# Kernel tuning notes

Hardware: AMD Instinct MI355X
Metric: run time of the kernel (lower is better)

The kernel has to match this reference:

```python
import jax, jax.numpy as jnp
import numpy as np

D_MODEL = 1024
D_STATE = 16
EXPAND = 2
D_INNER = EXPAND * D_MODEL
DT_RANK = 64  # ceil(1024/16)
D_CONV = 4


def setup_inputs() -> dict:
    key = jax.random.key(0)
    ks = jax.random.split(key, 8)
    s = 0.02
    x = jax.random.normal(ks[0], (2, 2048, D_MODEL), dtype=jnp.float32)
    W_in = jax.random.normal(ks[1], (D_MODEL, 2 * D_INNER), dtype=jnp.float32) * s
    W_conv = jax.random.normal(ks[2], (D_CONV, D_INNER), dtype=jnp.float32) * s  # depthwise taps
    b_conv = jnp.zeros((D_INNER,), dtype=jnp.float32)
    W_xproj = jax.random.normal(ks[3], (D_INNER, DT_RANK + 2 * D_STATE), dtype=jnp.float32) * s
    W_dt = jax.random.normal(ks[4], (DT_RANK, D_INNER), dtype=jnp.float32) * s
    b_dt = jnp.zeros((D_INNER,), dtype=jnp.float32)
    A_log = jnp.broadcast_to(jnp.log(jnp.arange(1, D_STATE + 1, dtype=jnp.float32)), (D_INNER, D_STATE))
    D = jnp.ones((D_INNER,), dtype=jnp.float32)
    W_out = jax.random.normal(ks[5], (D_INNER, D_MODEL), dtype=jnp.float32) * s
    return {"x": x, "W_in": W_in, "W_conv": W_conv, "b_conv": b_conv,
            "W_xproj": W_xproj, "W_dt": W_dt, "b_dt": b_dt,
            "A_log": A_log, "D": D, "W_out": W_out}


def _silu(v):
    return v * jax.nn.sigmoid(v)


def reference(x, W_in, W_conv, b_conv, W_xproj, W_dt, b_dt, A_log, D, W_out):
    B_, L, _ = x.shape
    xz = x @ W_in                     # [B, L, 2*d_inner]
    x_in, z = jnp.split(xz, 2, axis=-1)
    # causal depthwise conv1d (torch padding=d_conv-1 then slice to seq_len)
    pad = D_CONV - 1
    x_pad = jnp.pad(x_in, ((0, 0), (pad, 0), (0, 0)))
    x_conv = b_conv
    x_conv = sum(x_pad[:, k:k + L, :] * W_conv[k] for k in range(D_CONV)) + b_conv
    x_in = _silu(x_conv)              # [B, L, d_inner]
    dbc = x_in @ W_xproj
    dt = jax.nn.softplus(dbc[..., :DT_RANK] @ W_dt + b_dt)   # [B, L, d_inner]
    Bm = dbc[..., DT_RANK:DT_RANK + D_STATE]                  # [B, L, d_state]
    Cm = dbc[..., DT_RANK + D_STATE:]                          # [B, L, d_state]
    A = -jnp.exp(A_log)                                        # [d_inner, d_state]

    def step(state, inp):
        x_t, dt_t, B_t, C_t = inp   # [B,d_inner], [B,d_inner], [B,d_state], [B,d_state]
        dA = jnp.exp(jnp.clip(dt_t[:, :, None] * A[None], -10.0, 10.0))
        dB = dt_t[:, :, None] * B_t[:, None, :]
        state = jnp.clip(state * dA + x_t[:, :, None] * dB, -10.0, 10.0)
        y_t = jnp.einsum('bdn,bn->bd', state, C_t) + D * x_t
        return state, y_t

    tm = lambda a: jnp.swapaxes(a, 0, 1)  # time-major
    state0 = jnp.zeros((B_, D_INNER, D_STATE), dtype=x.dtype)
    _, ys = jax.lax.scan(step, state0, (tm(x_in), tm(dt), tm(Bm), tm(Cm)))
    y = jnp.swapaxes(ys, 0, 1)            # [B, L, d_inner]
    y = y * _silu(z)
    return y @ W_out                       # [B, L, d_model]
```

## Files before the change

kernel.cpp:

```cpp
#include <hip/hip_runtime.h>
#include <math.h>

#define D_MODEL 1024
#define D_INNER 2048
#define D_STATE 16
#define DT_RANK 64
#define LSEQ 2048
#define NBATCH 2
#define M_TOT (NBATCH * LSEQ)
#define DBC_STRIDE 128
#define CH 64
#define NCH (LSEQ / CH)
#define KSPL 8
#define OKSPL 2

typedef unsigned short ushort_t;
typedef unsigned int uint_t;
typedef __attribute__((ext_vector_type(8))) short bf16x8;
typedef __attribute__((ext_vector_type(4))) float f32x4;

__device__ __forceinline__ ushort_t f2bf_rne(float f) {
    uint_t u = __float_as_uint(f);
    u += 0x7fffu + ((u >> 16) & 1u);
    return (ushort_t)(u >> 16);
}
__device__ __forceinline__ float bf2f(ushort_t h) {
    return __uint_as_float(((uint_t)h) << 16);
}
__device__ __forceinline__ float fexp2(float x) {
#if __has_builtin(__builtin_amdgcn_exp2f)
    return __builtin_amdgcn_exp2f(x);
#else
    return exp2f(x);
#endif
}
__device__ __forceinline__ float frcp(float x) {
#if __has_builtin(__builtin_amdgcn_rcpf)
    return __builtin_amdgcn_rcpf(x);
#else
    return 1.f / x;
#endif
}
__device__ __forceinline__ float clip10(float x) {
#if __has_builtin(__builtin_amdgcn_fmed3f)
    return __builtin_amdgcn_fmed3f(x, -10.f, 10.f);
#else
    return fminf(fmaxf(x, -10.f), 10.f);
#endif
}

#define LOG2E 1.44269504f
#define NLOG2E10 -14.4269504f

#define KIN 1024
#define KTI (KIN / 64)

#define BAR()   __builtin_amdgcn_s_barrier()
#define LGKM0() asm volatile("s_waitcnt lgkmcnt(0)" ::: "memory")

#define LDFRAG_B(SRC)                                                          \
    _Pragma("unroll")                                                          \
    for (int nf = 0; nf < 4; ++nf)                                             \
        fB[nf] = *reinterpret_cast<const bf16x8*>(                             \
            &(SRC)[(bRow + nf * 16 + fm) * 32 + swz * 8]);

#define LDFRAG_A(SRC, MOFF)                                                    \
    _Pragma("unroll")                                                          \
    for (int mf = 0; mf < 4; ++mf)                                             \
        fA[mf] = *reinterpret_cast<const bf16x8*>(                             \
            &(SRC)[(aRow + (MOFF + mf) * 16 + fm) * 32 + swz * 8]);

#define MFMA_QUAD(MOFF)                                                        \
    __builtin_amdgcn_s_setprio(1);                                             \
    _Pragma("unroll")                                                          \
    for (int mf = 0; mf < 4; ++mf)                                             \
        _Pragma("unroll")                                                      \
        for (int nf = 0; nf < 4; ++nf)                                         \
            acc[MOFF + mf][nf] = __builtin_amdgcn_mfma_f32_16x16x32_bf16(      \
                fA[mf], fB[nf], acc[MOFF + mf][nf], 0, 0, 0);                  \
    __builtin_amdgcn_s_setprio(0);

__global__ __launch_bounds__(512, 2) void gemm256_inproj(
    const ushort_t* __restrict__ Ah, const ushort_t* __restrict__ BTh,
    float* __restrict__ C, float* __restrict__ AUX)
{
    __shared__ __align__(1024) ushort_t smem[65536];
    const int tid  = threadIdx.x;
    const int lane = tid & 63;
    const int w    = tid >> 6;
    const int wm   = w >> 2;
    const int wn   = w & 3;
    const int fm   = lane & 15, fk = lane >> 4;
    const int swz  = fk ^ ((fm >> 1) & 3);
    const int aRow = wm * 128;
    const int bRow = wn * 64;
    const int m0   = blockIdx.y * 256;
    const int n0   = blockIdx.x * 256;
    const int rbase = w * 16 + (lane >> 2);
    const int ssw   = ((lane & 3) ^ ((lane >> 3) & 3)) * 8;

    f32x4 acc[8][4] = {};

    auto stage = [&](const ushort_t* __restrict__ g, int grow0, int kcol,
                     int regUS) {
        #pragma unroll
        for (int q = 0; q < 2; ++q) {
            const ushort_t* src =
                g + (size_t)(grow0 + q * 128 + rbase) * KIN + kcol + ssw;
            __builtin_amdgcn_global_load_lds(
                (const __attribute__((address_space(1))) void*)src,
                (__attribute__((address_space(3))) void*)(smem + regUS +
                                                          q * 4096 + w * 512),
                16, 0, 0);
        }
    };

    stage(Ah,  m0, 0,  0);
    stage(BTh, n0, 0,  32768);
    stage(Ah,  m0, 32, 8192);
    stage(BTh, n0, 32, 32768 + 8192);
    stage(Ah,  m0, 64, 16384);
    stage(BTh, n0, 64, 32768 + 16384);
    asm volatile("s_waitcnt vmcnt(8)" ::: "memory");
    BAR();

    bf16x8 fA[4], fB[4];

    for (int t = 0; t < KTI - 1; ++t) {
        const int bf = t & 1, bn = bf ^ 1;
        const ushort_t* A0 = smem + (bf * 2 + 0) * 8192;
        const ushort_t* A1 = smem + (bf * 2 + 1) * 8192;
        const ushort_t* B0 = smem + 32768 + (bf * 2 + 0) * 8192;
        const ushort_t* B1 = smem + 32768 + (bf * 2 + 1) * 8192;
        const int kc1 = (t + 1) * 64, kc2 = (t + 2) * 64;
        const bool st2 = (t + 2 < KTI);

        LDFRAG_B(B0);
        LDFRAG_A(A0, 0);
        stage(Ah, m0, kc1 + 32, (bn * 2 + 1) * 8192);
        BAR(); LGKM0();
        MFMA_QUAD(0);
        BAR();

        LDFRAG_A(A0, 4);
        stage(BTh, n0, kc1 + 32, 32768 + (bn * 2 + 1) * 8192);
        BAR(); LGKM0();
        MFMA_QUAD(4);
        asm volatile("s_waitcnt vmcnt(8)" ::: "memory");
        BAR();
        __builtin_amdgcn_sched_barrier(0);

        LDFRAG_B(B1);
        LDFRAG_A(A1, 0);
        if (st2) stage(Ah, m0, kc2, (bf * 2 + 0) * 8192);
        BAR(); LGKM0();
        MFMA_QUAD(0);
        BAR();

        LDFRAG_A(A1, 4);
        if (st2) stage(BTh, n0, kc2, 32768 + (bf * 2 + 0) * 8192);
        BAR(); LGKM0();
        MFMA_QUAD(4);
        if (t == KTI - 2) { asm volatile("s_waitcnt vmcnt(4)" ::: "memory"); }
        else              { asm volatile("s_waitcnt vmcnt(6)" ::: "memory"); }
        BAR();
        __builtin_amdgcn_sched_barrier(0);
    }

    {
        const int bf = (KTI - 1) & 1;
        const ushort_t* A0 = smem + (bf * 2 + 0) * 8192;
        const ushort_t* A1 = smem + (bf * 2 + 1) * 8192;
        const ushort_t* B0 = smem + 32768 + (bf * 2 + 0) * 8192;
        const ushort_t* B1 = smem + 32768 + (bf * 2 + 1) * 8192;

        LDFRAG_B(B0);
        LDFRAG_A(A0, 0);
        BAR(); LGKM0();
        MFMA_QUAD(0);
        BAR();

        LDFRAG_A(A0, 4);
        BAR(); LGKM0();
        MFMA_QUAD(4);
        asm volatile("s_waitcnt vmcnt(0)" ::: "memory");
        BAR();

        LDFRAG_B(B1);
        LDFRAG_A(A1, 0);
        BAR(); LGKM0();
        MFMA_QUAD(0);
        BAR();

        LDFRAG_A(A1, 4);
        BAR(); LGKM0();
        MFMA_QUAD(4);
    }

    float* dst = (n0 < D_INNER) ? C : AUX;
    const int csub = (n0 < D_INNER) ? 0 : D_INNER;
    #pragma unroll
    for (int mf = 0; mf < 8; ++mf) {
        int row0 = m0 + aRow + mf * 16 + fk * 4;
        #pragma unroll
        for (int nf = 0; nf < 4; ++nf) {
            int col = n0 + bRow + nf * 16 + fm - csub;
            #pragma unroll
            for (int r = 0; r < 4; ++r)
                dst[(size_t)(row0 + r) * D_INNER + col] = acc[mf][nf][r];
        }
    }
}

template <int MODE, int TERMS>
__global__ __launch_bounds__(256) void gemm_bf16s(
    const ushort_t* __restrict__ Ah, const ushort_t* __restrict__ Al,
    const ushort_t* __restrict__ BTh, const ushort_t* __restrict__ BTl,
    float* __restrict__ C, float* __restrict__ AUX, int M, int N, int K)
{
    __shared__ __align__(16) ushort_t smem[4 * 128 * 32];
    ushort_t* sAh = smem;
    ushort_t* sAl = smem + 4096;
    ushort_t* sBh = smem + 8192;
    ushort_t* sBl = smem + 12288;
    const int tid = threadIdx.x;
    const int lane = tid & 63;
    const int m0 = blockIdx.y * 128;
    int ks = 0, nblk = blockIdx.x;
    if (MODE == 3) { ks = blockIdx.x; nblk = 0; }
    if (MODE == 4) { ks = blockIdx.x >> 3; nblk = blockIdx.x & 7; }
    const int n0 = nblk * 128;
    const int wave = tid >> 6;
    const int mw = (wave & 1) * 64, nw = (wave >> 1) * 64;
    const int fm = lane & 15, fk = lane >> 4;
    const int swz = fk ^ ((fm >> 1) & 3);

    f32x4 acc[4][4] = {};

    const int r_st0 = tid >> 2, cp0 = tid & 3;
    const int r_st1 = (256 + tid) >> 2, cp1 = tid & 3;
    const int cl0 = cp0 ^ ((r_st0 >> 1) & 3);
    const int cl1 = cp1 ^ ((r_st1 >> 1) & 3);
    const int ldsb0 = (tid & ~63) * 16;
    const int ldsb1 = (256 + (tid & ~63)) * 16;

    const int kbeg = (MODE == 3) ? ks * (K / KSPL)
                   : (MODE == 4) ? ks * (K / OKSPL) : 0;
    const int kend = (MODE == 3) ? kbeg + K / KSPL
                   : (MODE == 4) ? kbeg + K / OKSPL : K;

    for (int k0 = kbeg; k0 < kend; k0 += 32) {
        __syncthreads();
        {
            size_t ga0 = (size_t)(m0 + r_st0) * K + k0 + cl0 * 8;
            size_t ga1 = (size_t)(m0 + r_st1) * K + k0 + cl1 * 8;
            size_t gb0 = (size_t)(n0 + r_st0) * K + k0 + cl0 * 8;
            size_t gb1 = (size_t)(n0 + r_st1) * K + k0 + cl1 * 8;
            __builtin_amdgcn_global_load_lds(
                (const __attribute__((address_space(1))) void*)(Ah + ga0),
                (__attribute__((address_space(3))) void*)((char*)sAh + ldsb0), 16, 0, 0);
            __builtin_amdgcn_global_load_lds(
                (const __attribute__((address_space(1))) void*)(Ah + ga1),
                (__attribute__((address_space(3))) void*)((char*)sAh + ldsb1), 16, 0, 0);
            if (TERMS >= 3) {
                __builtin_amdgcn_global_load_lds(
                    (const __attribute__((address_space(1))) void*)(Al + ga0),
                    (__attribute__((address_space(3))) void*)((char*)sAl + ldsb0), 16, 0, 0);
                __builtin_amdgcn_global_load_lds(
                    (const __attribute__((address_space(1))) void*)(Al + ga1),
                    (__attribute__((address_space(3))) void*)((char*)sAl + ldsb1), 16, 0, 0);
            }
            __builtin_amdgcn_global_load_lds(
                (const __attribute__((address_space(1))) void*)(BTh + gb0),
                (__attribute__((address_space(3))) void*)((char*)sBh + ldsb0), 16, 0, 0);
            __builtin_amdgcn_global_load_lds(
                (const __attribute__((address_space(1))) void*)(BTh + gb1),
                (__attribute__((address_space(3))) void*)((char*)sBh + ldsb1), 16, 0, 0);
            if (TERMS >= 2) {
                __builtin_amdgcn_global_load_lds(
                    (const __attribute__((address_space(1))) void*)(BTl + gb0),
                    (__attribute__((address_space(3))) void*)((char*)sBl + ldsb0), 16, 0, 0);
                __builtin_amdgcn_global_load_lds(
                    (const __attribute__((address_space(1))) void*)(BTl + gb1),
                    (__attribute__((address_space(3))) void*)((char*)sBl + ldsb1), 16, 0, 0);
            }
        }
        __syncthreads();

        bf16x8 fAh[4], fAl[4], fBh[4], fBl[4];
        #pragma unroll
        for (int t = 0; t < 4; ++t) {
            int ra = (mw + t * 16 + fm) * 32 + swz * 8;
            int rb = (nw + t * 16 + fm) * 32 + swz * 8;
            fAh[t] = *reinterpret_cast<const bf16x8*>(&sAh[ra]);
            if (TERMS >= 3) fAl[t] = *reinterpret_cast<const bf16x8*>(&sAl[ra]);
            fBh[t] = *reinterpret_cast<const bf16x8*>(&sBh[rb]);
            if (TERMS >= 2) fBl[t] = *reinterpret_cast<const bf16x8*>(&sBl[rb]);
        }
        #pragma unroll
        for (int i = 0; i < 4; ++i)
            #pragma unroll
            for (int j = 0; j < 4; ++j) {
                acc[i][j] = __builtin_amdgcn_mfma_f32_16x16x32_bf16(fAh[i], fBh[j], acc[i][j], 0, 0, 0);
                if (TERMS >= 3)
                    acc[i][j] = __builtin_amdgcn_mfma_f32_16x16x32_bf16(fAl[i], fBh[j], acc[i][j], 0, 0, 0);
                if (TERMS >= 2)
                    acc[i][j] = __builtin_amdgcn_mfma_f32_16x16x32_bf16(fAh[i], fBl[j], acc[i][j], 0, 0, 0);
            }
    }

    float* Cq = (MODE == 3 || MODE == 4) ? C + (size_t)ks * M * N : C;
    #pragma unroll
    for (int i = 0; i < 4; ++i) {
        int row0 = m0 + mw + i * 16 + fk * 4;
        #pragma unroll
        for (int j = 0; j < 4; ++j) {
            int col = n0 + nw + j * 16 + fm;
            if (MODE == 5) {
                const float* bias = (const float*)AUX;
                float bc_ = bias[col];
                #pragma unroll
                for (int r = 0; r < 4; ++r) {
                    float t = acc[i][j][r] + bc_;
                    C[(size_t)(row0 + r) * N + col] =
                        fmaxf(t, 0.f) + log1pf(__expf(-fabsf(t)));
                }
            } else {
                #pragma unroll
                for (int r = 0; r < 4; ++r)
                    Cq[(size_t)(row0 + r) * N + col] = acc[i][j][r];
            }
        }
    }
}

__global__ __launch_bounds__(256) void xproj_red_k(
    const float* __restrict__ dbcp, float* __restrict__ dbc,
    ushort_t* __restrict__ dbch)
{
    int g = blockIdx.x * 256 + threadIdx.x;
    int m = g >> 7, c = g & 127;
    float s = 0.f;
    #pragma unroll
    for (int ks = 0; ks < KSPL; ++ks)
        s += dbcp[(size_t)ks * M_TOT * DBC_STRIDE + g];
    dbc[g] = s;
    if (c < 64)
        dbch[(size_t)m * 64 + c] = f2bf_rne(s);
}

__global__ __launch_bounds__(256) void outred_k(
    const float* __restrict__ p, float* __restrict__ out)
{
    int i4 = (blockIdx.x * 256 + threadIdx.x) * 4;
    f32x4 a = *reinterpret_cast<const f32x4*>(p + i4);
    f32x4 b = *reinterpret_cast<const f32x4*>(p + (size_t)M_TOT * D_MODEL + i4);
    *reinterpret_cast<f32x4*>(out + i4) = a + b;
}

__global__ __launch_bounds__(256) void cast_h_k(
    const float* __restrict__ X, ushort_t* __restrict__ Xh)
{
    int i4 = (blockIdx.x * 256 + threadIdx.x) * 4;
    float4 v = *reinterpret_cast<const float4*>(X + i4);
    ushort2 a = make_ushort2(f2bf_rne(v.x), f2bf_rne(v.y));
    ushort2 b = make_ushort2(f2bf_rne(v.z), f2bf_rne(v.w));
    *reinterpret_cast<ushort2*>(Xh + i4)     = a;
    *reinterpret_cast<ushort2*>(Xh + i4 + 2) = b;
}

__global__ __launch_bounds__(256) void transpose_cast_k(
    const float* __restrict__ W, ushort_t* __restrict__ Th, ushort_t* __restrict__ Tl,
    int K, int N)
{
    __shared__ float tile[32][33];
    int n0 = blockIdx.x * 32, k0 = blockIdx.y * 32;
    int tx = threadIdx.x & 31, ty = threadIdx.x >> 5;
    #pragma unroll
    for (int i = 0; i < 32; i += 8)
        tile[ty + i][tx] = W[(size_t)(k0 + ty + i) * N + n0 + tx];
    __syncthreads();
    #pragma unroll
    for (int i = 0; i < 32; i += 8) {
        float v = tile[tx][ty + i];
        ushort_t h = f2bf_rne(v);
        ushort_t l = f2bf_rne(v - bf2f(h));
        size_t o = (size_t)(n0 + ty + i) * K + k0 + tx;
        Th[o] = h; Tl[o] = l;
    }
}

__global__ __launch_bounds__(256) void transpose_cast_pad_k(
    const float* __restrict__ W, ushort_t* __restrict__ Th, int K, int N)
{
    __shared__ float tile[32][33];
    int n0 = blockIdx.x * 32, k0 = blockIdx.y * 32;
    int tx = threadIdx.x & 31, ty = threadIdx.x >> 5;
    #pragma unroll
    for (int i = 0; i < 32; i += 8)
        tile[ty + i][tx] = (n0 + tx < N) ? W[(size_t)(k0 + ty + i) * N + n0 + tx] : 0.f;
    __syncthreads();
    #pragma unroll
    for (int i = 0; i < 32; i += 8) {
        float v = tile[tx][ty + i];
        size_t o = (size_t)(n0 + ty + i) * K + k0 + tx;
        Th[o] = f2bf_rne(v);
    }
}

__global__ __launch_bounds__(256) void conv_silu_k(
    const float* __restrict__ xbuf, const float* __restrict__ Wc,
    const float* __restrict__ bc, ushort_t* __restrict__ xinh,
    float* __restrict__ xf)
{
    __shared__ float tile[67][64];
    const int c0 = blockIdx.x * 64;
    const int m0 = blockIdx.y * 64;
    const int bstart = m0 & ~(LSEQ - 1);
    const int tid = threadIdx.x;

    for (int e = tid; e < 67 * 64; e += 256) {
        int r = e >> 6, c = e & 63;
        int g = m0 - 3 + r;
        tile[r][c] = (g >= bstart) ? xbuf[(size_t)g * D_INNER + c0 + c] : 0.f;
    }
    __syncthreads();

    const int c_l = tid & 63, mg = tid >> 6;
    const int c = c0 + c_l;
    const float w0 = Wc[c], w1 = Wc[D_INNER + c];
    const float w2 = Wc[2 * D_INNER + c], w3 = Wc[3 * D_INNER + c];
    const float bb = bc[c];
    #pragma unroll
    for (int mi = 0; mi < 16; ++mi) {
        int r = mg * 16 + mi;
        float acc = bb + tile[r][c_l] * w0 + tile[r + 1][c_l] * w1
                       + tile[r + 2][c_l] * w2 + tile[r + 3][c_l] * w3;
        float sv = acc / (1.f + __expf(-acc));
        xinh[(size_t)(m0 + r) * D_INNER + c] = f2bf_rne(sv);
        xf[(size_t)(m0 + r) * D_INNER + c] = sv;
    }
}

__global__ __launch_bounds__(256) void scan_sum_k2(
    const float* __restrict__ dtf, const float* __restrict__ xf,
    const float* __restrict__ dbc, const float* __restrict__ A_log,
    float* __restrict__ asumb, float* __restrict__ sendb)
{
    __shared__ float sdt[16][256];
    __shared__ float sx[16][256];
    __shared__ float sB[16][16];
    const int tid = threadIdx.x;
    const int lane = tid & 63;
    const int w = tid >> 6;
    const int c0 = blockIdx.x << 8;
    const int ck = blockIdx.y;
    const int b  = blockIdx.z;
    const size_t mbase = (size_t)b * LSEQ + (size_t)ck * CH;
    const int d = c0 + tid;

    float AdnL2[16];
    #pragma unroll
    for (int n = 0; n < 16; ++n)
        AdnL2[n] = -__expf(A_log[d * D_STATE + n]) * LOG2E;

    float s[16] = {};
    float asum[16] = {};

    for (int tt = 0; tt < CH / 16; ++tt) {
        const size_t rowm = mbase + tt * 16;
        __syncthreads();
        #pragma unroll
        for (int p = 0; p < 4; ++p) {
            const int r = w + p * 4;
            const size_t g = (rowm + r) * D_INNER + c0 + lane * 4;
            __builtin_amdgcn_global_load_lds(
                (const __attribute__((address_space(1))) void*)(dtf + g),
                (__attribute__((address_space(3))) void*)(&sdt[r][0]), 16, 0, 0);
            __builtin_amdgcn_global_load_lds(
                (const __attribute__((address_space(1))) void*)(xf + g),
                (__attribute__((address_space(3))) void*)(&sx[r][0]), 16, 0, 0);
        }
        if (w == 0) {
            const int r = lane >> 2, c4 = (lane & 3) * 4;
            __builtin_amdgcn_global_load_lds(
                (const __attribute__((address_space(1))) void*)(
                    dbc + (rowm + r) * DBC_STRIDE + 64 + c4),
                (__attribute__((address_space(3))) void*)(&sB[0][0]), 16, 0, 0);
        }
        __syncthreads();

        #pragma unroll 2
        for (int t = 0; t < 16; ++t) {
            const float dv = sdt[t][tid];
            const float xv = sx[t][tid];
            const float p  = dv * xv;
            const f32x4 B0 = *reinterpret_cast<const f32x4*>(&sB[t][0]);
            const f32x4 B1 = *reinterpret_cast<const f32x4*>(&sB[t][4]);
            const f32x4 B2 = *reinterpret_cast<const f32x4*>(&sB[t][8]);
            const f32x4 B3 = *reinterpret_cast<const f32x4*>(&sB[t][12]);
            #pragma unroll
            for (int n = 0; n < 16; ++n) {
                const float Bn = (n < 4) ? B0[n] : (n < 8) ? B1[n - 4]
                               : (n < 12) ? B2[n - 8] : B3[n - 12];
                float a = fmaxf(dv * AdnL2[n], NLOG2E10);
                asum[n] += a;
                float e = fexp2(a);
                s[n] = clip10(fmaf(s[n], e, p * Bn));
            }
        }
    }
    #pragma unroll
    for (int n = 0; n < 16; ++n) {
        size_t o = (((size_t)(b * NCH + ck) * 16) + n) * D_INNER + d;
        asumb[o] = asum[n];
        sendb[o] = s[n];
    }
}

__global__ __launch_bounds__(256) void scan_fix_k2(
    const float* __restrict__ asumb, const float* __restrict__ sendb,
    float* __restrict__ sinb)
{
    int g = blockIdx.x * 256 + threadIdx.x;
    int d = g & (D_INNER - 1);
    int n = (g >> 11) & 15;
    int b = g >> 15;
    float s = 0.f;
    for (int ck = 0; ck < NCH; ++ck) {
        size_t idx = (((size_t)(b * NCH + ck) * 16) + n) * D_INNER + d;
        sinb[idx] = s;
        s = clip10(fmaf(s, fexp2(asumb[idx]), sendb[idx]));
    }
}

__global__ __launch_bounds__(256) void scan_apply_k2(
    const float* __restrict__ dtf, const float* __restrict__ xf,
    const float* __restrict__ dbc, const float* __restrict__ zf,
    const float* __restrict__ sinb, const float* __restrict__ A_log,
    const float* __restrict__ Dv, ushort_t* __restrict__ Yh)
{
    __shared__ float sdt[16][256];
    __shared__ float sx[16][256];
    __shared__ float sz[16][256];
    __shared__ float sBC[16][32];
    const int tid = threadIdx.x;
    const int lane = tid & 63;
    const int w = tid >> 6;
    const int c0 = blockIdx.x << 8;
    const int ck = blockIdx.y;
    const int b  = blockIdx.z;
    const size_t mbase = (size_t)b * LSEQ + (size_t)ck * CH;
    const int d = c0 + tid;

    float AdnL2[16];
    #pragma unroll
    for (int n = 0; n < 16; ++n)
        AdnL2[n] = -__expf(A_log[d * D_STATE + n]) * LOG2E;
    const float Dd = Dv[d];

    float s[16];
    #pragma unroll
    for (int n = 0; n < 16; ++n)
        s[n] = sinb[(((size_t)(b * NCH + ck) * 16) + n) * D_INNER + d];

    for (int tt = 0; tt < CH / 16; ++tt) {
        const size_t rowm = mbase + tt * 16;
        __syncthreads();
        #pragma unroll
        for (int p = 0; p < 4; ++p) {
            const int r = w + p * 4;
            const size_t g = (rowm + r) * D_INNER + c0 + lane * 4;
            __builtin_amdgcn_global_load_lds(
                (const __attribute__((address_space(1))) void*)(dtf + g),
                (__attribute__((address_space(3))) void*)(&sdt[r][0]), 16, 0, 0);
            __builtin_amdgcn_global_load_lds(
                (const __attribute__((address_space(1))) void*)(xf + g),
                (__attribute__((address_space(3))) void*)(&sx[r][0]), 16, 0, 0);
            __builtin_amdgcn_global_load_lds(
                (const __attribute__((address_space(1))) void*)(zf + g),
                (__attribute__((address_space(3))) void*)(&sz[r][0]), 16, 0, 0);
        }
        if (w < 2) {
            const int r = tid >> 3, c8 = (tid & 7) * 4;
            __builtin_amdgcn_global_load_lds(
                (const __attribute__((address_space(1))) void*)(
                    dbc + (rowm + r) * DBC_STRIDE + 64 + c8),
                (__attribute__((address_space(3))) void*)(&sBC[w * 8][0]), 16, 0, 0);
        }
        __syncthreads();

        #pragma unroll 2
        for (int t = 0; t < 16; ++t) {
            const float dv = sdt[t][tid];
            const float xv = sx[t][tid];
            const float p  = dv * xv;
            const f32x4 B0 = *reinterpret_cast<const f32x4*>(&sBC[t][0]);
            const f32x4 B1 = *reinterpret_cast<const f32x4*>(&sBC[t][4]);
            const f32x4 B2 = *reinterpret_cast<const f32x4*>(&sBC[t][8]);
            const f32x4 B3 = *reinterpret_cast<const f32x4*>(&sBC[t][12]);
            const f32x4 C0 = *reinterpret_cast<const f32x4*>(&sBC[t][16]);
            const f32x4 C1 = *reinterpret_cast<const f32x4*>(&sBC[t][20]);
            const f32x4 C2 = *reinterpret_cast<const f32x4*>(&sBC[t][24]);
            const f32x4 C3 = *reinterpret_cast<const f32x4*>(&sBC[t][28]);
            float y = Dd * xv;
            #pragma unroll
            for (int n = 0; n < 16; ++n) {
                const float Bn = (n < 4) ? B0[n] : (n < 8) ? B1[n - 4]
                               : (n < 12) ? B2[n - 8] : B3[n - 12];
                const float Cn = (n < 4) ? C0[n] : (n < 8) ? C1[n - 4]
                               : (n < 12) ? C2[n - 8] : C3[n - 12];
                float a = fmaxf(dv * AdnL2[n], NLOG2E10);
                float e = fexp2(a);
                s[n] = clip10(fmaf(s[n], e, p * Bn));
                y = fmaf(s[n], Cn, y);
            }
            const float zz = sz[t][tid];
            const float gate = zz * frcp(1.f + fexp2(zz * -LOG2E));
            Yh[(rowm + t) * D_INNER + d] = f2bf_rne(y * gate);
        }
    }
}

extern "C" void kernel_launch(void* const* d_in, const int* in_sizes, int n_in,
                              void* d_out, int out_size, void* d_ws, size_t ws_size,
                              hipStream_t stream)
{
    const float* x       = (const float*)d_in[0];
    const float* W_in    = (const float*)d_in[1];
    const float* W_conv  = (const float*)d_in[2];
    const float* b_conv  = (const float*)d_in[3];
    const float* W_xproj = (const float*)d_in[4];
    const float* W_dt    = (const float*)d_in[5];
    const float* b_dt    = (const float*)d_in[6];
    const float* A_log   = (const float*)d_in[7];
    const float* Dv      = (const float*)d_in[8];
    const float* W_out   = (const float*)d_in[9];
    float* out = (float*)d_out;

    float* xbuf = (float*)d_ws;
    float* zf   = xbuf + (size_t)M_TOT * D_INNER;
    float* dbc  = zf + (size_t)M_TOT * D_INNER;
    float* BCT  = dbc + (size_t)M_TOT * DBC_STRIDE;
    ushort_t* xh     = (ushort_t*)(BCT + (size_t)32 * M_TOT);
    ushort_t* xl     = xh + (size_t)M_TOT * D_MODEL;
    ushort_t* WinTh  = xl + (size_t)M_TOT * D_MODEL;
    ushort_t* WinTl  = WinTh + (size_t)2 * D_INNER * D_MODEL;
    ushort_t* WoutTh = WinTl + (size_t)2 * D_INNER * D_MODEL;
    ushort_t* WoutTl = WoutTh + (size_t)D_MODEL * D_INNER;
    ushort_t* WxTh   = WoutTl + (size_t)D_MODEL * D_INNER;
    ushort_t* WxTl   = WxTh + (size_t)DBC_STRIDE * D_INNER;
    ushort_t* xinh   = WxTl + (size_t)DBC_STRIDE * D_INNER;
    ushort_t* xinl   = xinh + (size_t)M_TOT * D_INNER;
    ushort_t* yh     = xinl + (size_t)M_TOT * D_INNER;
    ushort_t* yl     = yh + (size_t)M_TOT * D_INNER;
    ushort_t* WdtTh  = yl + (size_t)M_TOT * D_INNER;
    ushort_t* dbch   = WdtTh + (size_t)D_INNER * DT_RANK;
    float* xf   = (float*)xh;
    float* dtf  = (float*)xinh;
    float* dbcp = (float*)yh;
    float* pout = (float*)xh;
    const size_t NSUM = (size_t)NBATCH * NCH * D_INNER * D_STATE;
    float* asumb = xbuf;
    float* sendb = xbuf + NSUM;
    float* sinb  = xbuf + 2 * NSUM;

    cast_h_k<<<(M_TOT * D_MODEL) / 1024, 256, 0, stream>>>(x, xh);
    transpose_cast_pad_k<<<dim3((2 * D_INNER) / 32, D_MODEL / 32), 256, 0, stream>>>(
        W_in, WinTh, D_MODEL, 2 * D_INNER);
    transpose_cast_k<<<dim3(D_MODEL / 32, D_INNER / 32), 256, 0, stream>>>(
        W_out, WoutTh, WoutTl, D_INNER, D_MODEL);
    transpose_cast_pad_k<<<dim3(DBC_STRIDE / 32, D_INNER / 32), 256, 0, stream>>>(
        W_xproj, WxTh, D_INNER, DT_RANK + 2 * D_STATE);
    transpose_cast_pad_k<<<dim3(D_INNER / 32, DT_RANK / 32), 256, 0, stream>>>(
        W_dt, WdtTh, DT_RANK, D_INNER);

    gemm256_inproj<<<dim3(16, 16), 512, 0, stream>>>(xh, WinTh, xbuf, zf);
    conv_silu_k<<<dim3(D_INNER / 64, M_TOT / 64), 256, 0, stream>>>(
        xbuf, W_conv, b_conv, xinh, xf);
    gemm_bf16s<3, 1><<<dim3(KSPL, 32), 256, 0, stream>>>(
        xinh, nullptr, WxTh, nullptr, dbcp, nullptr, M_TOT, DBC_STRIDE, D_INNER);
    xproj_red_k<<<(M_TOT * DBC_STRIDE) / 256, 256, 0, stream>>>(dbcp, dbc, dbch);
    gemm_bf16s<5, 1><<<dim3(D_INNER / 128, M_TOT / 128), 256, 0, stream>>>(
        dbch, nullptr, WdtTh, nullptr, dtf, (float*)b_dt, M_TOT, D_INNER, DT_RANK);
    scan_sum_k2<<<dim3(D_INNER / 256, NCH, NBATCH), 256, 0, stream>>>(
        dtf, xf, dbc, A_log, asumb, sendb);
    scan_fix_k2<<<(NBATCH * D_STATE * D_INNER) / 256, 256, 0, stream>>>(
        asumb, sendb, sinb);
    scan_apply_k2<<<dim3(D_INNER / 256, NCH, NBATCH), 256, 0, stream>>>(
        dtf, xf, dbc, zf, sinb, A_log, Dv, yh);
    gemm_bf16s<4, 2><<<dim3(OKSPL * 8, 32), 256, 0, stream>>>(
        yh, nullptr, WoutTh, WoutTl, pout, nullptr, M_TOT, D_MODEL, D_INNER);
    outred_k<<<(M_TOT * D_MODEL) / 1024, 256, 0, stream>>>(pout, out);
}
```

Measured before the change: 347.3 us.

## Replace out-projection GEMM with 256x128 double-buffered pipelined 512-thread kernel

Swaps the generic 128x128 split-K bf16 GEMM for the output projection with a dedicated 512-thread kernel modeled on the in-projection kernel. It uses 256x128 tiles, double-buffered LDS staging via global_load_lds, explicit vmcnt waits and barriers, and MFMA priority hints. The hi/lo split of W_out is kept for accuracy. The goal is better overlap of loads with MFMA and more reuse per tile, at the cost of a large LDS footprint and hand-tuned wait counts that must be exactly right.

Result: faster. 340.2 us (-2.0%).

```diff
diff --git a/kernel.cpp b/kernel.cpp
--- a/kernel.cpp
+++ b/kernel.cpp
@@ -52,9 +52,6 @@
 #define LOG2E 1.44269504f
 #define NLOG2E10 -14.4269504f
 
-#define KIN 1024
-#define KTI (KIN / 64)
-
 #define BAR()   __builtin_amdgcn_s_barrier()
 #define LGKM0() asm volatile("s_waitcnt lgkmcnt(0)" ::: "memory")
 
@@ -79,6 +76,9 @@
             acc[MOFF + mf][nf] = __builtin_amdgcn_mfma_f32_16x16x32_bf16(      \
                 fA[mf], fB[nf], acc[MOFF + mf][nf], 0, 0, 0);                  \
     __builtin_amdgcn_s_setprio(0);
+
+#define KIN 1024
+#define KTI (KIN / 64)
 
 __global__ __launch_bounds__(512, 2) void gemm256_inproj(
     const ushort_t* __restrict__ Ah, const ushort_t* __restrict__ BTh,
@@ -212,6 +212,158 @@
     }
 }
 
+#define KOUT 2048
+#define NTOUT 16
+
+__global__ __launch_bounds__(512, 2) void gemm256_outproj(
+    const ushort_t* __restrict__ Ah, const ushort_t* __restrict__ BTh,
+    const ushort_t* __restrict__ BTl, float* __restrict__ P)
+{
+    __shared__ __align__(1024) ushort_t smem[65536];
+    const int tid  = threadIdx.x;
+    const int lane = tid & 63;
+    const int w    = tid >> 6;
+    const int wm   = w & 3;
+    const int wn   = w >> 2;
+    const int fm   = lane & 15, fk = lane >> 4;
+    const int swz  = fk ^ ((fm >> 1) & 3);
+    const int aRow = wm * 64;
+    const int bRow = wn * 64;
+    const int ks   = blockIdx.x >> 3;
+    const int n0   = (blockIdx.x & 7) * 128;
+    const int m0   = blockIdx.y * 256;
+    const int kb   = ks * (KOUT / OKSPL);
+    const int rbase = w * 16 + (lane >> 2);
+    const int ssw   = ((lane & 3) ^ ((lane >> 3) & 3)) * 8;
+
+    f32x4 acc[4][4] = {};
+
+    auto stageA = [&](int t, int kh) {
+        const int kcol = kb + t * 64 + kh * 32;
+        const int reg = ((t & 1) * 2 + kh) * 8192;
+        #pragma unroll
+        for (int q = 0; q < 2; ++q) {
+            const ushort_t* src =
+                Ah + (size_t)(m0 + q * 128 + rbase) * KOUT + kcol + ssw;
+            __builtin_amdgcn_global_load_lds(
+                (const __attribute__((address_space(1))) void*)src,
+                (__attribute__((address_space(3))) void*)(smem + reg +
+                                                          q * 4096 + w * 512),
+                16, 0, 0);
+        }
+    };
+    auto stageB = [&](const ushort_t* __restrict__ B, int base, int t, int kh) {
+        const int kcol = kb + t * 64 + kh * 32;
+        const int reg = base + ((t & 1) * 2 + kh) * 4096;
+        const ushort_t* src = B + (size_t)(n0 + rbase) * KOUT + kcol + ssw;
+        __builtin_amdgcn_global_load_lds(
+            (const __attribute__((address_space(1))) void*)src,
+            (__attribute__((address_space(3))) void*)(smem + reg + w * 512),
+            16, 0, 0);
+    };
+
+    stageA(0, 0);
+    stageA(0, 1);
+    stageB(BTh, 32768, 0, 0);
+    stageB(BTh, 32768, 0, 1);
+    stageB(BTl, 49152, 0, 0);
+    stageB(BTl, 49152, 0, 1);
+    asm volatile("s_waitcnt vmcnt(3)" ::: "memory");
+    BAR();
+
+    bf16x8 fA[4], fB[4];
+
+    for (int t = 0; t < NTOUT - 1; ++t) {
+        const int bf = t & 1;
+        const ushort_t* A0  = smem + (bf * 2 + 0) * 8192;
+        const ushort_t* A1  = smem + (bf * 2 + 1) * 8192;
+        const ushort_t* Bh0 = smem + 32768 + (bf * 2 + 0) * 4096;
+        const ushort_t* Bh1 = smem + 32768 + (bf * 2 + 1) * 4096;
+        const ushort_t* Bl0 = smem + 49152 + (bf * 2 + 0) * 4096;
+        const ushort_t* Bl1 = smem + 49152 + (bf * 2 + 1) * 4096;
+
+        LDFRAG_B(Bh0);
+        LDFRAG_A(A0, 0);
+        stageA(t + 1, 0);
+        BAR(); LGKM0();
+        MFMA_QUAD(0);
+        asm volatile("s_waitcnt vmcnt(3)" ::: "memory");
+        BAR();
+        __builtin_amdgcn_sched_barrier(0);
+
+        LDFRAG_B(Bl0);
+        stageA(t + 1, 1);
+        BAR(); LGKM0();
+        MFMA_QUAD(0);
+        BAR();
+
+        LDFRAG_B(Bh1);
+        LDFRAG_A(A1, 0);
+        stageB(BTh, 32768, t + 1, 0);
+        stageB(BTh, 32768, t + 1, 1);
+        BAR(); LGKM0();
+        MFMA_QUAD(0);
+        asm volatile("s_waitcnt vmcnt(6)" ::: "memory");
+        BAR();
+        __builtin_amdgcn_sched_barrier(0);
+
+        LDFRAG_B(Bl1);
+        stageB(BTl, 49152, t + 1, 0);
+        stageB(BTl, 49152, t + 1, 1);
+        BAR(); LGKM0();
+        MFMA_QUAD(0);
+        asm volatile("s_waitcnt vmcnt(3)" ::: "memory");
+        BAR();
+        __builtin_amdgcn_sched_barrier(0);
+    }
+
+    {
+        const int bf = (NTOUT - 1) & 1;
+        const ushort_t* A0  = smem + (bf * 2 + 0) * 8192;
+        const ushort_t* A1  = smem + (bf * 2 + 1) * 8192;
+        const ushort_t* Bh0 = smem + 32768 + (bf * 2 + 0) * 4096;
+        const ushort_t* Bh1 = smem + 32768 + (bf * 2 + 1) * 4096;
+        const ushort_t* Bl0 = smem + 49152 + (bf * 2 + 0) * 4096;
+        const ushort_t* Bl1 = smem + 49152 + (bf * 2 + 1) * 4096;
+
+        LDFRAG_B(Bh0);
+        LDFRAG_A(A0, 0);
+        BAR(); LGKM0();
+        MFMA_QUAD(0);
+        asm volatile("s_waitcnt vmcnt(1)" ::: "memory");
+        BAR();
+
+        LDFRAG_B(Bl0);
+        BAR(); LGKM0();
+        MFMA_QUAD(0);
+        BAR();
+
+        LDFRAG_B(Bh1);
+        LDFRAG_A(A1, 0);
+        BAR(); LGKM0();
+        MFMA_QUAD(0);
+        asm volatile("s_waitcnt vmcnt(0)" ::: "memory");
+        BAR();
+
+        LDFRAG_B(Bl1);
+        BAR(); LGKM0();
+        MFMA_QUAD(0);
+    }
+
+    float* Pq = P + (size_t)ks * M_TOT * D_MODEL;
+    #pragma unroll
+    for (int mf = 0; mf < 4; ++mf) {
+        int row0 = m0 + aRow + mf * 16 + fk * 4;
+        #pragma unroll
+        for (int nf = 0; nf < 4; ++nf) {
+            int col = n0 + bRow + nf * 16 + fm;
+            #pragma unroll
+            for (int r = 0; r < 4; ++r)
+                Pq[(size_t)(row0 + r) * D_MODEL + col] = acc[mf][nf][r];
+        }
+    }
+}
+
 template <int MODE, int TERMS>
 __global__ __launch_bounds__(256) void gemm_bf16s(
     const ushort_t* __restrict__ Ah, const ushort_t* __restrict__ Al,
@@ -228,7 +380,6 @@
     const int m0 = blockIdx.y * 128;
     int ks = 0, nblk = blockIdx.x;
     if (MODE == 3) { ks = blockIdx.x; nblk = 0; }
-    if (MODE == 4) { ks = blockIdx.x >> 3; nblk = blockIdx.x & 7; }
     const int n0 = nblk * 128;
     const int wave = tid >> 6;
     const int mw = (wave & 1) * 64, nw = (wave >> 1) * 64;
@@ -244,10 +395,8 @@
     const int ldsb0 = (tid & ~63) * 16;
     const int ldsb1 = (256 + (tid & ~63)) * 16;
 
-    const int kbeg = (MODE == 3) ? ks * (K / KSPL)
-                   : (MODE == 4) ? ks * (K / OKSPL) : 0;
-    const int kend = (MODE == 3) ? kbeg + K / KSPL
-                   : (MODE == 4) ? kbeg + K / OKSPL : K;
+    const int kbeg = (MODE == 3) ? ks * (K / KSPL) : 0;
+    const int kend = (MODE == 3) ? kbeg + K / KSPL : K;
 
     for (int k0 = kbeg; k0 < kend; k0 += 32) {
         __syncthreads();
@@ -309,7 +458,7 @@
             }
     }
 
-    float* Cq = (MODE == 3 || MODE == 4) ? C + (size_t)ks * M * N : C;
+    float* Cq = (MODE == 3) ? C + (size_t)ks * M * N : C;
     #pragma unroll
     for (int i = 0; i < 4; ++i) {
         int row0 = m0 + mw + i * 16 + fk * 4;
@@ -689,7 +838,6 @@
         asumb, sendb, sinb);
     scan_apply_k2<<<dim3(D_INNER / 256, NCH, NBATCH), 256, 0, stream>>>(
         dtf, xf, dbc, zf, sinb, A_log, Dv, yh);
-    gemm_bf16s<4, 2><<<dim3(OKSPL * 8, 32), 256, 0, stream>>>(
-        yh, nullptr, WoutTh, WoutTl, pout, nullptr, M_TOT, D_MODEL, D_INNER);
+    gemm256_outproj<<<dim3(16, 16), 512, 0, stream>>>(yh, WoutTh, WoutTl, pout);
     outred_k<<<(M_TOT * D_MODEL) / 1024, 256, 0, stream>>>(pout, out);
 }
```
